# Optimization experiments

Hardware: AMD Instinct MI355X
Metric: run time of the kernel (lower is better)

The kernel has to match this reference:

```python
import jax, jax.numpy as jnp
import numpy as np
import math

DIMS, K_SIZE, V_SIZE = 1024, 128, 128

def setup_inputs() -> dict:
    key = jax.random.key(0)
    ks = jax.random.split(key, 7)
    B, S = 4, 2048
    scale = 1.0 / math.sqrt(DIMS)
    return {
        "inputs": jax.random.normal(ks[0], (B, S, DIMS), dtype=jnp.float32),
        "Wq": jax.random.normal(ks[1], (DIMS, K_SIZE), dtype=jnp.float32) * scale,
        "bq": jnp.zeros((K_SIZE,), dtype=jnp.float32),
        "Wk": jax.random.normal(ks[2], (DIMS, K_SIZE), dtype=jnp.float32) * scale,
        "bk": jnp.zeros((K_SIZE,), dtype=jnp.float32),
        "Wv": jax.random.normal(ks[3], (DIMS, V_SIZE), dtype=jnp.float32) * scale,
        "bv": jnp.zeros((V_SIZE,), dtype=jnp.float32),
    }

def reference(inputs, Wq, bq, Wk, bk, Wv, bv):
    # inputs: [B, S, D]
    q = inputs @ Wq + bq            # [B, S, k]
    k = inputs @ Wk + bk            # [B, S, k]
    v = inputs @ Wv + bv            # [B, S, v]
    logits = jnp.einsum('bqk,bsk->bqs', q, k)  # [B, S, S]
    S = inputs.shape[1]
    causal = jnp.tril(jnp.ones((S, S), dtype=bool))  # allow j <= i (triu k=1 masked)
    logits = jnp.where(causal, logits, -jnp.inf)
    probs = jax.nn.softmax(logits / jnp.sqrt(jnp.float32(Wk.shape[1])), axis=-1)
    read = jnp.einsum('bqs,bsv->bqv', probs, v)  # [B, S, v]
    return jnp.concatenate([inputs, read], axis=-1)  # [B, S, D+v]
```

## Files before the change

kernel.cpp:

```cpp
#include <hip/hip_runtime.h>
#include <hip/hip_bf16.h>

typedef __attribute__((ext_vector_type(8))) short bf16x8;
typedef __attribute__((ext_vector_type(4))) float f32x4;
typedef __attribute__((ext_vector_type(4))) unsigned short u16x4;
typedef __attribute__((ext_vector_type(4))) float float4_t;

static constexpr int Bn = 4, Sn = 2048, Dn = 1024, Kn = 128;
static constexpr int ODn = Dn + Kn;
static constexpr int CPB = 80;
static constexpr float L2E = 1.4426950408889634f;

__device__ __forceinline__ unsigned short f2bf(float f) {
    union { float f; unsigned int u; } v; v.f = f;
    unsigned int u = v.u;
    return (unsigned short)((u + 0x7fffu + ((u >> 16) & 1u)) >> 16);
}

#define GLOAD16(g, l) __builtin_amdgcn_global_load_lds( \
    (const __attribute__((address_space(1))) void*)(g), \
    (__attribute__((address_space(3))) void*)(l), 16, 0, 0)

__global__ __launch_bounds__(256) void wt_prep(const float* __restrict__ Wq,
                                               const float* __restrict__ Wk,
                                               const float* __restrict__ Wv,
                                               unsigned short* __restrict__ Wt) {
    __shared__ unsigned short tile[32][34];
    int k0 = blockIdx.x * 32, c0 = blockIdx.y * 32, w = blockIdx.z;
    const float* W = (w == 0) ? Wq : (w == 1) ? Wk : Wv;
    int tc = threadIdx.x & 31;
    int tr = (threadIdx.x >> 5) * 4;
#pragma unroll
    for (int i = 0; i < 4; ++i)
        tile[tr + i][tc] = f2bf(W[(size_t)(k0 + tr + i) * Kn + c0 + tc]);
    __syncthreads();
    unsigned short* dst = Wt + (size_t)w * Kn * Dn;
#pragma unroll
    for (int i = 0; i < 4; ++i)
        dst[(size_t)(c0 + tr + i) * Dn + k0 + tc] = tile[tc][tr + i];
}

__global__ __launch_bounds__(256, 2) void proj_kernel(
    const float* __restrict__ X, const unsigned short* __restrict__ Wt,
    const float* __restrict__ bq, const float* __restrict__ bk, const float* __restrict__ bv,
    float* __restrict__ out,
    unsigned short* __restrict__ qws, unsigned short* __restrict__ kws,
    unsigned short* __restrict__ vtws) {
    __shared__ __align__(16) unsigned short Alds[2][32 * 32];
    __shared__ __align__(16) unsigned short Wlds[2][384 * 32];
    const int m0 = blockIdx.x * 32;
    const int t = threadIdx.x;
    const int lane = t & 63, wn = t >> 6;
    const int lr = lane & 15, lg = lane >> 4;
    const int arow = t >> 3, af4 = t & 7;

    const unsigned short* wsrc[6];
#pragma unroll
    for (int p = 0; p < 6; ++p) {
        int col = wn * 96 + p * 16 + (lane >> 2);
        int seg = lane & 3;
        wsrc[p] = Wt + (size_t)col * Dn + seg * 8;
    }
    f32x4 acc[2][6] = {};

    {
        float4_t av = *(const float4_t*)(X + (size_t)(m0 + arow) * Dn + af4 * 4);
#pragma unroll
        for (int p = 0; p < 6; ++p)
            GLOAD16(wsrc[p], (char*)&Wlds[0][0] + wn * 6144 + p * 1024);
        *(float4_t*)(out + (size_t)(m0 + arow) * ODn + af4 * 4) = av;
        u16x4 hv;
        hv[0] = f2bf(av[0]); hv[1] = f2bf(av[1]); hv[2] = f2bf(av[2]); hv[3] = f2bf(av[3]);
        *(u16x4*)((char*)&Alds[0][0] + arow * 64 + af4 * 8) = hv;
    }
    __syncthreads();

    for (int k0 = 0; k0 < Dn; k0 += 32) {
        const int cur = (k0 >> 5) & 1;
        const int kn = k0 + 32;
        float4_t avn = {};
        if (kn < Dn) {
            avn = *(const float4_t*)(X + (size_t)(m0 + arow) * Dn + kn + af4 * 4);
#pragma unroll
            for (int p = 0; p < 6; ++p)
                GLOAD16(wsrc[p] + kn, (char*)&Wlds[cur ^ 1][0] + wn * 6144 + p * 1024);
        }
        bf16x8 afr[2], bfr[6];
#pragma unroll
        for (int mi = 0; mi < 2; ++mi)
            afr[mi] = *(const bf16x8*)((const char*)&Alds[cur][0] + (mi * 16 + lr) * 64 + lg * 16);
#pragma unroll
        for (int ni = 0; ni < 6; ++ni)
            bfr[ni] = *(const bf16x8*)((const char*)&Wlds[cur][0] + (wn * 96 + ni * 16 + lr) * 64 + lg * 16);
        __builtin_amdgcn_s_setprio(1);
#pragma unroll
        for (int mi = 0; mi < 2; ++mi)
#pragma unroll
            for (int ni = 0; ni < 6; ++ni)
                acc[mi][ni] = __builtin_amdgcn_mfma_f32_16x16x32_bf16(afr[mi], bfr[ni], acc[mi][ni], 0, 0, 0);
        __builtin_amdgcn_s_setprio(0);
        if (kn < Dn) {
            *(float4_t*)(out + (size_t)(m0 + arow) * ODn + kn + af4 * 4) = avn;
            u16x4 hv;
            hv[0] = f2bf(avn[0]); hv[1] = f2bf(avn[1]); hv[2] = f2bf(avn[2]); hv[3] = f2bf(avn[3]);
            *(u16x4*)((char*)&Alds[cur ^ 1][0] + arow * 64 + af4 * 8) = hv;
        }
        __syncthreads();
    }
#pragma unroll
    for (int ni = 0; ni < 6; ++ni) {
        int gcol = wn * 96 + ni * 16 + lr;
        int buf = gcol >> 7, ci = gcol & 127;
        float bias = (buf == 0 ? bq : buf == 1 ? bk : bv)[ci];
#pragma unroll
        for (int mi = 0; mi < 2; ++mi) {
#pragma unroll
            for (int r = 0; r < 4; ++r) {
                int grow = m0 + mi * 16 + lg * 4 + r;
                unsigned short hv = f2bf(acc[mi][ni][r] + bias);
                if (buf == 0) qws[(size_t)grow * Kn + ci] = hv;
                else if (buf == 1) kws[(size_t)grow * Kn + ci] = hv;
                else {
                    int bb = grow >> 11, ss = grow & 2047;
                    vtws[((size_t)bb * Kn + ci) * Sn + ss] = hv;
                }
            }
        }
    }
}

__global__ __launch_bounds__(256, 2) void attn_kernel(
    const unsigned short* __restrict__ qws, const unsigned short* __restrict__ kws,
    const unsigned short* __restrict__ vtws,
    float* __restrict__ part_o, float* __restrict__ part_ml) {
    __shared__ __align__(16) unsigned short Klds[2][64 * 128];
    __shared__ __align__(16) unsigned short Vlds[2][128 * 64];
    __shared__ __align__(16) unsigned short Plds[4][16 * 64];
    constexpr float SCALE = 0.08838834764831845f;
    const int t = threadIdx.x, lane = t & 63, wid = t >> 6;
    const int lr = lane & 15, lg = lane >> 4;
    const int pidx = blockIdx.x;
    const int b = pidx / CPB;
    const int idx = pidx - b * CPB;
    int qt, c;
    if (idx < 8)       { qt = idx;                c = 0; }
    else if (idx < 24) { int r = idx - 8;  qt = 8  + (r >> 1); c = r & 1; }
    else if (idx < 48) { int r = idx - 24; int q3 = r / 3; qt = 16 + q3; c = r - q3 * 3; }
    else               { int r = idx - 48; qt = 24 + (r >> 2); c = r & 3; }
    const int it0 = c * 8;
    const int it1 = (c * 8 + 8 < qt + 1) ? (c * 8 + 8) : (qt + 1);
    const int qrow0 = qt * 64 + wid * 16;

    const unsigned short* kb  = kws  + (size_t)b * Sn * Kn;
    const unsigned short* vtb = vtws + (size_t)b * Kn * Sn;
    const unsigned short* ksrc[4];
    const unsigned short* vsrc[4];
#pragma unroll
    for (int p = 0; p < 4; ++p) {
        int row = wid * 16 + p * 4 + (lane >> 4);
        int seg = lane & 15;
        ksrc[p] = kb + (size_t)row * Kn + ((seg ^ (row & 7)) * 8);
        int cc = wid * 32 + p * 8 + (lane >> 3);
        int sg = lane & 7;
        vsrc[p] = vtb + (size_t)cc * Sn + ((sg ^ (cc & 7)) * 8);
    }
    auto stage = [&](int buf, int it) {
#pragma unroll
        for (int p = 0; p < 4; ++p) {
            GLOAD16(ksrc[p] + (size_t)it * (64 * Kn), (char*)&Klds[buf][0] + wid * 4096 + p * 1024);
            GLOAD16(vsrc[p] + (size_t)it * 64,        (char*)&Vlds[buf][0] + wid * 4096 + p * 1024);
        }
    };

    const unsigned short* qbase = qws + ((size_t)b * Sn + qrow0) * Kn;
    bf16x8 qf[4];
#pragma unroll
    for (int kk = 0; kk < 4; ++kk)
        qf[kk] = *(const bf16x8*)(qbase + (size_t)lr * Kn + kk * 32 + lg * 8);
    f32x4 o[8] = {};
    float mrow[4] = {-1e30f, -1e30f, -1e30f, -1e30f};
    float lrow[4] = {0.f, 0.f, 0.f, 0.f};

    stage(0, it0);
    __syncthreads();

    for (int it = it0; it < it1; ++it) {
        const int cur = (it - it0) & 1;
        if (it + 1 < it1) stage(cur ^ 1, it + 1);
        const int kv0 = it * 64;
        f32x4 s[4] = {};
        __builtin_amdgcn_s_setprio(1);
#pragma unroll
        for (int n = 0; n < 4; ++n) {
            int kvr = n * 16 + lr;
#pragma unroll
            for (int kk = 0; kk < 4; ++kk) {
                int off = (kvr * 256 + kk * 64 + lg * 16) ^ ((kvr & 7) << 4);
                bf16x8 kf = *(const bf16x8*)((const char*)&Klds[cur][0] + off);
                s[n] = __builtin_amdgcn_mfma_f32_16x16x32_bf16(qf[kk], kf, s[n], 0, 0, 0);
            }
        }
        __builtin_amdgcn_s_setprio(0);
#pragma unroll
        for (int n = 0; n < 4; ++n) {
            int kvg = kv0 + n * 16 + lr;
#pragma unroll
            for (int r = 0; r < 4; ++r) {
                float sv = s[n][r] * SCALE;
                int qg = qrow0 + lg * 4 + r;
                s[n][r] = (kvg > qg) ? -1e30f : sv;
            }
        }
        float tmax[4], rsum[4], alpha[4];
#pragma unroll
        for (int r = 0; r < 4; ++r)
            tmax[r] = fmaxf(fmaxf(s[0][r], s[1][r]), fmaxf(s[2][r], s[3][r]));
#pragma unroll
        for (int d = 1; d < 16; d <<= 1)
#pragma unroll
            for (int r = 0; r < 4; ++r)
                tmax[r] = fmaxf(tmax[r], __shfl_xor(tmax[r], d));
#pragma unroll
        for (int r = 0; r < 4; ++r) {
            float mnew = fmaxf(mrow[r], tmax[r]);
            alpha[r] = exp2f((mrow[r] - mnew) * L2E);
            mrow[r] = mnew;
            rsum[r] = 0.f;
        }
        unsigned short pb[4][4];
#pragma unroll
        for (int n = 0; n < 4; ++n)
#pragma unroll
            for (int r = 0; r < 4; ++r) {
                float p = exp2f((s[n][r] - mrow[r]) * L2E);
                rsum[r] += p;
                pb[n][r] = f2bf(p);
            }
#pragma unroll
        for (int d = 1; d < 16; d <<= 1)
#pragma unroll
            for (int r = 0; r < 4; ++r)
                rsum[r] += __shfl_xor(rsum[r], d);
#pragma unroll
        for (int r = 0; r < 4; ++r)
            lrow[r] = lrow[r] * alpha[r] + rsum[r];
#pragma unroll
        for (int v = 0; v < 8; ++v)
#pragma unroll
            for (int r = 0; r < 4; ++r)
                o[v][r] *= alpha[r];
        char* pbase = (char*)&Plds[wid][0];
#pragma unroll
        for (int n = 0; n < 4; ++n)
#pragma unroll
            for (int r = 0; r < 4; ++r) {
                int q = lg * 4 + r, kv = n * 16 + lr;
                int off = (q * 128 + kv * 2) ^ ((q & 7) << 4);
                *(unsigned short*)(pbase + off) = pb[n][r];
            }
        bf16x8 pa[2];
#pragma unroll
        for (int kk = 0; kk < 2; ++kk) {
            int aoff = (lr * 128 + kk * 64 + lg * 16) ^ ((lr & 7) << 4);
            pa[kk] = *(const bf16x8*)((const char*)pbase + aoff);
        }
        __builtin_amdgcn_s_setprio(1);
#pragma unroll
        for (int v = 0; v < 8; ++v) {
            int vcol = v * 16 + lr;
#pragma unroll
            for (int kk = 0; kk < 2; ++kk) {
                int boff = (vcol * 128 + kk * 64 + lg * 16) ^ ((vcol & 7) << 4);
                bf16x8 vb = *(const bf16x8*)((const char*)&Vlds[cur][0] + boff);
                o[v] = __builtin_amdgcn_mfma_f32_16x16x32_bf16(pa[kk], vb, o[v], 0, 0, 0);
            }
        }
        __builtin_amdgcn_s_setprio(0);
        __syncthreads();
    }
    const size_t pbo = (size_t)pidx * (64 * 128);
#pragma unroll
    for (int v = 0; v < 8; ++v)
#pragma unroll
        for (int r = 0; r < 4; ++r) {
            int row = wid * 16 + lg * 4 + r;
            part_o[pbo + (size_t)row * 128 + v * 16 + lr] = o[v][r];
        }
    if (lr == 0) {
#pragma unroll
        for (int r = 0; r < 4; ++r) {
            int row = wid * 16 + lg * 4 + r;
            part_ml[(size_t)pidx * 128 + row * 2]     = mrow[r];
            part_ml[(size_t)pidx * 128 + row * 2 + 1] = lrow[r];
        }
    }
}

__global__ __launch_bounds__(256) void reduce_kernel(
    const float* __restrict__ part_o, const float* __restrict__ part_ml,
    float* __restrict__ out) {
    const int bid = blockIdx.x;
    const int rh = bid & 1, bq = bid >> 1;
    const int qt = bq & 31, b = bq >> 5;
    const int g = qt >> 3, nch = g + 1;
    const int cum[4] = {0, 8, 24, 48};
    const int idx0 = cum[g] + (qt - (g << 3)) * nch;
    const int pidx0 = b * CPB + idx0;
    const int t = threadIdx.x;
    const int row = rh * 32 + (t >> 3);
    const int col0 = (t & 7) * 16;

    float mc[4], lc[4];
#pragma unroll
    for (int cc = 0; cc < 4; ++cc) { mc[cc] = -1e30f; lc[cc] = 0.f; }
#pragma unroll
    for (int cc = 0; cc < 4; ++cc)
        if (cc < nch) {
            mc[cc] = part_ml[(size_t)(pidx0 + cc) * 128 + row * 2];
            lc[cc] = part_ml[(size_t)(pidx0 + cc) * 128 + row * 2 + 1];
        }
    float m = fmaxf(fmaxf(mc[0], mc[1]), fmaxf(mc[2], mc[3]));
    float w[4], l = 0.f;
#pragma unroll
    for (int cc = 0; cc < 4; ++cc) {
        w[cc] = exp2f((mc[cc] - m) * L2E);
        l += w[cc] * lc[cc];
    }
    float4_t acc4[4] = {};
#pragma unroll
    for (int cc = 0; cc < 4; ++cc)
        if (cc < nch) {
            const float* po = part_o + (size_t)(pidx0 + cc) * (64 * 128) + (size_t)row * 128 + col0;
#pragma unroll
            for (int j = 0; j < 4; ++j) {
                float4_t v = *(const float4_t*)(po + j * 4);
                acc4[j] += v * w[cc];
            }
        }
    const float inv = 1.f / l;
    const size_t grow = (size_t)b * Sn + qt * 64 + row;
#pragma unroll
    for (int j = 0; j < 4; ++j)
        *(float4_t*)(out + grow * ODn + Dn + col0 + j * 4) = acc4[j] * inv;
}

extern "C" void kernel_launch(void* const* d_in, const int* in_sizes, int n_in,
                              void* d_out, int out_size, void* d_ws, size_t ws_size,
                              hipStream_t stream) {
    const float* X  = (const float*)d_in[0];
    const float* Wq = (const float*)d_in[1];
    const float* bq = (const float*)d_in[2];
    const float* Wk = (const float*)d_in[3];
    const float* bk = (const float*)d_in[4];
    const float* Wv = (const float*)d_in[5];
    const float* bv = (const float*)d_in[6];
    float* out = (float*)d_out;

    unsigned short* Wt   = (unsigned short*)d_ws;
    unsigned short* qws  = Wt  + (size_t)3 * Kn * Dn;
    unsigned short* kws  = qws + (size_t)Bn * Sn * Kn;
    unsigned short* vtws = kws + (size_t)Bn * Sn * Kn;
    float* part_o  = (float*)(vtws + (size_t)Bn * Sn * Kn);
    float* part_ml = part_o + (size_t)Bn * CPB * 64 * 128;

    wt_prep<<<dim3(32, 4, 3), 256, 0, stream>>>(Wq, Wk, Wv, Wt);
    proj_kernel<<<256, 256, 0, stream>>>(X, Wt, bq, bk, bv, out, qws, kws, vtws);
    attn_kernel<<<Bn * CPB, 256, 0, stream>>>(qws, kws, vtws, part_o, part_ml);
    reduce_kernel<<<256, 256, 0, stream>>>(part_o, part_ml, out);
}
```

Measured before the change: 78.72 us.

## Retile projection, split attention into smaller KV chunks, store partials in bf16

The projection kernel now gives each block a 64-row by 96-column tile instead of 32 rows by all 384 columns. It uses a 64-wide K step with XOR-swizzled LDS layouts and a grid of 512 blocks remapped across XCDs, and the fp32 copy of X is written by only one of the four column blocks. Attention work is split into chunks of 4 KV tiles (144 blocks per batch instead of 80) for better load balance. The causal mask is applied only on the diagonal tile. Attention partial outputs are stored as bf16 to halve reduce traffic, which costs some precision, and the reduce kernel is generalised to up to 8 chunks.

```diff
diff --git a/kernel.cpp b/kernel.cpp
--- a/kernel.cpp
+++ b/kernel.cpp
@@ -3,18 +3,23 @@
 
 typedef __attribute__((ext_vector_type(8))) short bf16x8;
 typedef __attribute__((ext_vector_type(4))) float f32x4;
-typedef __attribute__((ext_vector_type(4))) unsigned short u16x4;
+typedef __attribute__((ext_vector_type(8))) unsigned short u16x8;
 typedef __attribute__((ext_vector_type(4))) float float4_t;
 
 static constexpr int Bn = 4, Sn = 2048, Dn = 1024, Kn = 128;
 static constexpr int ODn = Dn + Kn;
-static constexpr int CPB = 80;
+static constexpr int CH = 4;
+static constexpr int CPB = 144;
 static constexpr float L2E = 1.4426950408889634f;
 
 __device__ __forceinline__ unsigned short f2bf(float f) {
     union { float f; unsigned int u; } v; v.f = f;
     unsigned int u = v.u;
     return (unsigned short)((u + 0x7fffu + ((u >> 16) & 1u)) >> 16);
+}
+__device__ __forceinline__ float bf2f(unsigned short h) {
+    union { float f; unsigned int u; } v; v.u = ((unsigned int)h) << 16;
+    return v.f;
 }
 
 #define GLOAD16(g, l) __builtin_amdgcn_global_load_lds( \
@@ -46,84 +51,98 @@
     float* __restrict__ out,
     unsigned short* __restrict__ qws, unsigned short* __restrict__ kws,
     unsigned short* __restrict__ vtws) {
-    __shared__ __align__(16) unsigned short Alds[2][32 * 32];
-    __shared__ __align__(16) unsigned short Wlds[2][384 * 32];
-    const int m0 = blockIdx.x * 32;
-    const int t = threadIdx.x;
-    const int lane = t & 63, wn = t >> 6;
+    __shared__ __align__(16) unsigned short Alds[2][64 * 64];
+    __shared__ __align__(16) unsigned short Wlds[2][96 * 64];
+    const int orig = blockIdx.x;
+    const int wg = (orig & 7) * 64 + (orig >> 3);
+    const int m0 = (wg >> 2) * 64;
+    const int ns = wg & 3;
+    const int c0 = ns * 96;
+    const int t = threadIdx.x, lane = t & 63, wn = t >> 6;
     const int lr = lane & 15, lg = lane >> 4;
-    const int arow = t >> 3, af4 = t & 7;
-
-    const unsigned short* wsrc[6];
-#pragma unroll
-    for (int p = 0; p < 6; ++p) {
-        int col = wn * 96 + p * 16 + (lane >> 2);
-        int seg = lane & 3;
-        wsrc[p] = Wt + (size_t)col * Dn + seg * 8;
-    }
-    f32x4 acc[2][6] = {};
-
-    {
-        float4_t av = *(const float4_t*)(X + (size_t)(m0 + arow) * Dn + af4 * 4);
-#pragma unroll
-        for (int p = 0; p < 6; ++p)
-            GLOAD16(wsrc[p], (char*)&Wlds[0][0] + wn * 6144 + p * 1024);
-        *(float4_t*)(out + (size_t)(m0 + arow) * ODn + af4 * 4) = av;
-        u16x4 hv;
-        hv[0] = f2bf(av[0]); hv[1] = f2bf(av[1]); hv[2] = f2bf(av[2]); hv[3] = f2bf(av[3]);
-        *(u16x4*)((char*)&Alds[0][0] + arow * 64 + af4 * 8) = hv;
-    }
+    const int ar0 = t >> 3, ach = t & 7;
+
+    const unsigned short* wsrcp[3]; int wdst[3];
+#pragma unroll
+    for (int p = 0; p < 3; ++p) {
+        int s = t + p * 256, col = s >> 3, kseg = s & 7;
+        wsrcp[p] = Wt + (size_t)(c0 + col) * Dn + ((kseg ^ (col & 7)) * 8);
+        wdst[p] = col * 128 + kseg * 16;
+    }
+    const float* xbase = X + (size_t)(m0 + ar0) * Dn + ach * 8;
+    float* obase = out + (size_t)(m0 + ar0) * ODn + ach * 8;
+    f32x4 acc[6] = {};
+    float4_t va[4];
+
+    auto loadA = [&](int k0) {
+        va[0] = *(const float4_t*)(xbase + k0);
+        va[1] = *(const float4_t*)(xbase + k0 + 4);
+        va[2] = *(const float4_t*)(xbase + (size_t)32 * Dn + k0);
+        va[3] = *(const float4_t*)(xbase + (size_t)32 * Dn + k0 + 4);
+    };
+    auto stageW = [&](int buf, int k0) {
+#pragma unroll
+        for (int p = 0; p < 3; ++p)
+            GLOAD16(wsrcp[p] + k0, (char*)&Wlds[buf][0] + wdst[p]);
+    };
+    auto writeA = [&](int buf, int k0) {
+        if ((k0 >> 8) == ns) {
+            *(float4_t*)(obase + k0) = va[0];
+            *(float4_t*)(obase + k0 + 4) = va[1];
+            *(float4_t*)(obase + (size_t)32 * ODn + k0) = va[2];
+            *(float4_t*)(obase + (size_t)32 * ODn + k0 + 4) = va[3];
+        }
+        u16x8 h0, h1;
+#pragma unroll
+        for (int j = 0; j < 4; ++j) {
+            h0[j] = f2bf(va[0][j]); h0[j + 4] = f2bf(va[1][j]);
+            h1[j] = f2bf(va[2][j]); h1[j + 4] = f2bf(va[3][j]);
+        }
+        const int r1 = ar0 + 32;
+        *(u16x8*)((char*)&Alds[buf][0] + ar0 * 128 + ((ach * 16) ^ ((ar0 & 7) << 4))) = h0;
+        *(u16x8*)((char*)&Alds[buf][0] + r1 * 128 + ((ach * 16) ^ ((r1 & 7) << 4))) = h1;
+    };
+
+    loadA(0); stageW(0, 0); writeA(0, 0);
     __syncthreads();
 
-    for (int k0 = 0; k0 < Dn; k0 += 32) {
-        const int cur = (k0 >> 5) & 1;
-        const int kn = k0 + 32;
-        float4_t avn = {};
-        if (kn < Dn) {
-            avn = *(const float4_t*)(X + (size_t)(m0 + arow) * Dn + kn + af4 * 4);
-#pragma unroll
-            for (int p = 0; p < 6; ++p)
-                GLOAD16(wsrc[p] + kn, (char*)&Wlds[cur ^ 1][0] + wn * 6144 + p * 1024);
-        }
-        bf16x8 afr[2], bfr[6];
-#pragma unroll
-        for (int mi = 0; mi < 2; ++mi)
-            afr[mi] = *(const bf16x8*)((const char*)&Alds[cur][0] + (mi * 16 + lr) * 64 + lg * 16);
-#pragma unroll
-        for (int ni = 0; ni < 6; ++ni)
-            bfr[ni] = *(const bf16x8*)((const char*)&Wlds[cur][0] + (wn * 96 + ni * 16 + lr) * 64 + lg * 16);
+    const int arow = wn * 16 + lr;
+    const int asw = (arow & 7) << 4;
+    for (int k0 = 0; k0 < Dn; k0 += 64) {
+        const int cur = (k0 >> 6) & 1;
+        const int kn = k0 + 64;
+        if (kn < Dn) { loadA(kn); stageW(cur ^ 1, kn); }
         __builtin_amdgcn_s_setprio(1);
 #pragma unroll
-        for (int mi = 0; mi < 2; ++mi)
-#pragma unroll
-            for (int ni = 0; ni < 6; ++ni)
-                acc[mi][ni] = __builtin_amdgcn_mfma_f32_16x16x32_bf16(afr[mi], bfr[ni], acc[mi][ni], 0, 0, 0);
+        for (int kk = 0; kk < 2; ++kk) {
+            bf16x8 afr = *(const bf16x8*)((const char*)&Alds[cur][0] +
+                          arow * 128 + ((kk * 64 + lg * 16) ^ asw));
+#pragma unroll
+            for (int ni = 0; ni < 6; ++ni) {
+                int col = ni * 16 + lr;
+                bf16x8 bfr = *(const bf16x8*)((const char*)&Wlds[cur][0] +
+                              col * 128 + ((kk * 64 + lg * 16) ^ ((col & 7) << 4)));
+                acc[ni] = __builtin_amdgcn_mfma_f32_16x16x32_bf16(afr, bfr, acc[ni], 0, 0, 0);
+            }
+        }
         __builtin_amdgcn_s_setprio(0);
-        if (kn < Dn) {
-            *(float4_t*)(out + (size_t)(m0 + arow) * ODn + kn + af4 * 4) = avn;
-            u16x4 hv;
-            hv[0] = f2bf(avn[0]); hv[1] = f2bf(avn[1]); hv[2] = f2bf(avn[2]); hv[3] = f2bf(avn[3]);
-            *(u16x4*)((char*)&Alds[cur ^ 1][0] + arow * 64 + af4 * 8) = hv;
-        }
+        if (kn < Dn) writeA(cur ^ 1, kn);
         __syncthreads();
     }
 #pragma unroll
     for (int ni = 0; ni < 6; ++ni) {
-        int gcol = wn * 96 + ni * 16 + lr;
+        int gcol = c0 + ni * 16 + lr;
         int buf = gcol >> 7, ci = gcol & 127;
         float bias = (buf == 0 ? bq : buf == 1 ? bk : bv)[ci];
 #pragma unroll
-        for (int mi = 0; mi < 2; ++mi) {
-#pragma unroll
-            for (int r = 0; r < 4; ++r) {
-                int grow = m0 + mi * 16 + lg * 4 + r;
-                unsigned short hv = f2bf(acc[mi][ni][r] + bias);
-                if (buf == 0) qws[(size_t)grow * Kn + ci] = hv;
-                else if (buf == 1) kws[(size_t)grow * Kn + ci] = hv;
-                else {
-                    int bb = grow >> 11, ss = grow & 2047;
-                    vtws[((size_t)bb * Kn + ci) * Sn + ss] = hv;
-                }
+        for (int r = 0; r < 4; ++r) {
+            int grow = m0 + wn * 16 + lg * 4 + r;
+            unsigned short hv = f2bf(acc[ni][r] + bias);
+            if (buf == 0) qws[(size_t)grow * Kn + ci] = hv;
+            else if (buf == 1) kws[(size_t)grow * Kn + ci] = hv;
+            else {
+                int bb = grow >> 11, ss = grow & 2047;
+                vtws[((size_t)bb * Kn + ci) * Sn + ss] = hv;
             }
         }
     }
@@ -132,7 +151,7 @@
 __global__ __launch_bounds__(256, 2) void attn_kernel(
     const unsigned short* __restrict__ qws, const unsigned short* __restrict__ kws,
     const unsigned short* __restrict__ vtws,
-    float* __restrict__ part_o, float* __restrict__ part_ml) {
+    unsigned short* __restrict__ part_o, float* __restrict__ part_ml) {
     __shared__ __align__(16) unsigned short Klds[2][64 * 128];
     __shared__ __align__(16) unsigned short Vlds[2][128 * 64];
     __shared__ __align__(16) unsigned short Plds[4][16 * 64];
@@ -142,13 +161,11 @@
     const int pidx = blockIdx.x;
     const int b = pidx / CPB;
     const int idx = pidx - b * CPB;
-    int qt, c;
-    if (idx < 8)       { qt = idx;                c = 0; }
-    else if (idx < 24) { int r = idx - 8;  qt = 8  + (r >> 1); c = r & 1; }
-    else if (idx < 48) { int r = idx - 24; int q3 = r / 3; qt = 16 + q3; c = r - q3 * 3; }
-    else               { int r = idx - 48; qt = 24 + (r >> 2); c = r & 3; }
-    const int it0 = c * 8;
-    const int it1 = (c * 8 + 8 < qt + 1) ? (c * 8 + 8) : (qt + 1);
+    int qt = 0, rem = idx;
+    while (true) { int n = (qt + CH) >> 2; if (rem < n) break; rem -= n; ++qt; }
+    const int c = rem;
+    const int it0 = c * CH;
+    const int it1 = (it0 + CH < qt + 1) ? (it0 + CH) : (qt + 1);
     const int qrow0 = qt * 64 + wid * 16;
 
     const unsigned short* kb  = kws  + (size_t)b * Sn * Kn;
@@ -201,15 +218,23 @@
             }
         }
         __builtin_amdgcn_s_setprio(0);
-#pragma unroll
-        for (int n = 0; n < 4; ++n) {
-            int kvg = kv0 + n * 16 + lr;
-#pragma unroll
-            for (int r = 0; r < 4; ++r) {
-                float sv = s[n][r] * SCALE;
-                int qg = qrow0 + lg * 4 + r;
-                s[n][r] = (kvg > qg) ? -1e30f : sv;
-            }
+        if (it == qt) {
+#pragma unroll
+            for (int n = 0; n < 4; ++n) {
+                int kvg = kv0 + n * 16 + lr;
+#pragma unroll
+                for (int r = 0; r < 4; ++r) {
+                    float sv = s[n][r] * SCALE;
+                    int qg = qrow0 + lg * 4 + r;
+                    s[n][r] = (kvg > qg) ? -1e30f : sv;
+                }
+            }
+        } else {
+#pragma unroll
+            for (int n = 0; n < 4; ++n)
+#pragma unroll
+                for (int r = 0; r < 4; ++r)
+                    s[n][r] *= SCALE;
         }
         float tmax[4], rsum[4], alpha[4];
 #pragma unroll
@@ -284,7 +309,7 @@
 #pragma unroll
         for (int r = 0; r < 4; ++r) {
             int row = wid * 16 + lg * 4 + r;
-            part_o[pbo + (size_t)row * 128 + v * 16 + lr] = o[v][r];
+            part_o[pbo + (size_t)row * 128 + v * 16 + lr] = f2bf(o[v][r]);
         }
     if (lr == 0) {
 #pragma unroll
@@ -297,51 +322,54 @@
 }
 
 __global__ __launch_bounds__(256) void reduce_kernel(
-    const float* __restrict__ part_o, const float* __restrict__ part_ml,
+    const unsigned short* __restrict__ part_o, const float* __restrict__ part_ml,
     float* __restrict__ out) {
     const int bid = blockIdx.x;
     const int rh = bid & 1, bq = bid >> 1;
     const int qt = bq & 31, b = bq >> 5;
-    const int g = qt >> 3, nch = g + 1;
-    const int cum[4] = {0, 8, 24, 48};
-    const int idx0 = cum[g] + (qt - (g << 3)) * nch;
+    const int nch = (qt + CH) >> 2;
+    int idx0 = 0;
+    for (int q = 0; q < qt; ++q) idx0 += (q + CH) >> 2;
     const int pidx0 = b * CPB + idx0;
     const int t = threadIdx.x;
     const int row = rh * 32 + (t >> 3);
     const int col0 = (t & 7) * 16;
 
-    float mc[4], lc[4];
-#pragma unroll
-    for (int cc = 0; cc < 4; ++cc) { mc[cc] = -1e30f; lc[cc] = 0.f; }
-#pragma unroll
-    for (int cc = 0; cc < 4; ++cc)
+    float mc[8], lc[8];
+#pragma unroll
+    for (int cc = 0; cc < 8; ++cc) { mc[cc] = -1e30f; lc[cc] = 0.f; }
+#pragma unroll
+    for (int cc = 0; cc < 8; ++cc)
         if (cc < nch) {
             mc[cc] = part_ml[(size_t)(pidx0 + cc) * 128 + row * 2];
             lc[cc] = part_ml[(size_t)(pidx0 + cc) * 128 + row * 2 + 1];
         }
-    float m = fmaxf(fmaxf(mc[0], mc[1]), fmaxf(mc[2], mc[3]));
-    float w[4], l = 0.f;
-#pragma unroll
-    for (int cc = 0; cc < 4; ++cc) {
-        w[cc] = exp2f((mc[cc] - m) * L2E);
-        l += w[cc] * lc[cc];
-    }
-    float4_t acc4[4] = {};
-#pragma unroll
-    for (int cc = 0; cc < 4; ++cc)
+    float m = -1e30f;
+#pragma unroll
+    for (int cc = 0; cc < 8; ++cc) m = fmaxf(m, mc[cc]);
+    float l = 0.f;
+    float accv[16] = {};
+#pragma unroll
+    for (int cc = 0; cc < 8; ++cc)
         if (cc < nch) {
-            const float* po = part_o + (size_t)(pidx0 + cc) * (64 * 128) + (size_t)row * 128 + col0;
-#pragma unroll
-            for (int j = 0; j < 4; ++j) {
-                float4_t v = *(const float4_t*)(po + j * 4);
-                acc4[j] += v * w[cc];
+            float w = exp2f((mc[cc] - m) * L2E);
+            l += w * lc[cc];
+            const unsigned short* po = part_o + (size_t)(pidx0 + cc) * (64 * 128) + (size_t)row * 128 + col0;
+            bf16x8 v0 = *(const bf16x8*)(po);
+            bf16x8 v1 = *(const bf16x8*)(po + 8);
+#pragma unroll
+            for (int j = 0; j < 8; ++j) {
+                accv[j]     += w * bf2f((unsigned short)v0[j]);
+                accv[8 + j] += w * bf2f((unsigned short)v1[j]);
             }
         }
     const float inv = 1.f / l;
-    const size_t grow = (size_t)b * Sn + qt * 64 + row;
-#pragma unroll
-    for (int j = 0; j < 4; ++j)
-        *(float4_t*)(out + grow * ODn + Dn + col0 + j * 4) = acc4[j] * inv;
+    float* op = out + ((size_t)b * Sn + qt * 64 + row) * ODn + Dn + col0;
+#pragma unroll
+    for (int j = 0; j < 4; ++j) {
+        float4_t v = { accv[j*4] * inv, accv[j*4+1] * inv, accv[j*4+2] * inv, accv[j*4+3] * inv };
+        *(float4_t*)(op + j * 4) = v;
+    }
 }
 
 extern "C" void kernel_launch(void* const* d_in, const int* in_sizes, int n_in,
@@ -360,11 +388,11 @@
     unsigned short* qws  = Wt  + (size_t)3 * Kn * Dn;
     unsigned short* kws  = qws + (size_t)Bn * Sn * Kn;
     unsigned short* vtws = kws + (size_t)Bn * Sn * Kn;
-    float* part_o  = (float*)(vtws + (size_t)Bn * Sn * Kn);
-    float* part_ml = part_o + (size_t)Bn * CPB * 64 * 128;
+    unsigned short* part_o = vtws + (size_t)Bn * Sn * Kn;
+    float* part_ml = (float*)(part_o + (size_t)Bn * CPB * 64 * 128);
 
     wt_prep<<<dim3(32, 4, 3), 256, 0, stream>>>(Wq, Wk, Wv, Wt);
-    proj_kernel<<<256, 256, 0, stream>>>(X, Wt, bq, bk, bv, out, qws, kws, vtws);
+    proj_kernel<<<512, 256, 0, stream>>>(X, Wt, bq, bk, bv, out, qws, kws, vtws);
     attn_kernel<<<Bn * CPB, 256, 0, stream>>>(qws, kws, vtws, part_o, part_ml);
     reduce_kernel<<<256, 256, 0, stream>>>(part_o, part_ml, out);
 }
```

After: 68.52 us. -13.0%, faster.
